# Performance work log

Hardware: AMD Instinct MI355X
Metric: run time of the kernel (lower is better)

## Reference

```python
import jax, jax.numpy as jnp
import numpy as np

R, H, E = 200000, 256, 100000  # num_relations, hidden_dim, num_hyperedges


def setup_inputs() -> dict:
    key = jax.random.key(0)
    ks = jax.random.split(key, 8)
    rng = np.random.default_rng(0)
    # ragged hyperedge sizes in [1, 15], avg ~8 -> total ~800k src entries
    sizes = rng.integers(1, 16, size=E)
    total = int(sizes.sum())
    he_ptr = jnp.asarray(np.concatenate([[0], np.cumsum(sizes)]), dtype=jnp.int64)
    he_src = jax.random.randint(ks[0], (total,), 0, R, dtype=jnp.int64)
    # unique targets make the scatter deterministic and equivalent)
    he_tgt = jnp.asarray(rng.permutation(R)[:E], dtype=jnp.int64)
    he_w = jax.random.uniform(ks[1], (E,), dtype=jnp.float32)
    x = jax.random.normal(ks[2], (R, H), dtype=jnp.float32)
    s = 1.0 / np.sqrt(H)
    W_msg = jax.random.uniform(ks[3], (H, H), jnp.float32, -s, s)
    b_msg = jnp.zeros((H,), jnp.float32)
    W_gate = jax.random.uniform(ks[4], (2 * H, H), jnp.float32, -s, s)
    b_gate = jnp.zeros((H,), jnp.float32)
    W_upd = jax.random.uniform(ks[5], (H, H), jnp.float32, -s, s)
    b_upd = jnp.zeros((H,), jnp.float32)
    return {"x": x, "he_ptr": he_ptr, "he_src": he_src, "he_tgt": he_tgt,
            "he_w": he_w, "W_msg": W_msg, "b_msg": b_msg,
            "W_gate": W_gate, "b_gate": b_gate, "W_upd": W_upd, "b_upd": b_upd}


def reference(x, he_ptr, he_src, he_tgt, he_w, W_msg, b_msg, W_gate, b_gate, W_upd, b_upd):
    total = he_src.shape[0]
    num_e = he_tgt.shape[0]
    # segment id of each src entry: which hyperedge it belongs to
    seg = jnp.searchsorted(he_ptr, jnp.arange(total), side="right") - 1
    gathered = x[he_src]                                   # [total, H]
    sums = jax.ops.segment_sum(gathered, seg, num_segments=num_e)  # [E, H]
    counts = (he_ptr[1:] - he_ptr[:-1]).astype(x.dtype)    # [E]
    src_mean = sums / counts[:, None]                      # segment mean
    msg = src_mean @ W_msg + b_msg                         # [E, H]
    tgt_x = x[he_tgt]                                      # [E, H]
    gate = jax.nn.sigmoid(jnp.concatenate([tgt_x, msg], axis=-1) @ W_gate + b_gate)
    upd = tgt_x + he_w[:, None] * gate * msg               # gated residual
    out = x.at[he_tgt].set(upd)                            # unique targets
    out = jnp.clip(out @ W_upd + b_upd, 0.0, 1.0)          # clipped relu
    return out
```

## Files before the change

kernel.cpp:

```cpp
#include <hip/hip_runtime.h>
#include <math.h>

#define H 256

typedef __attribute__((ext_vector_type(8))) short short8;
typedef __attribute__((ext_vector_type(4))) float f32x4;
typedef __attribute__((ext_vector_type(4))) int int4v;
typedef __attribute__((ext_vector_type(2))) unsigned int uint2v;
typedef unsigned short ushort_t;

__device__ __forceinline__ float bf2f(unsigned short u) {
    union { unsigned int i; float f; } v; v.i = ((unsigned int)u) << 16; return v.f;
}
__device__ __forceinline__ unsigned short f2bf(float f) {
    union { float f; unsigned int i; } v; v.f = f;
    unsigned int r = v.i + 0x7FFFu + ((v.i >> 16) & 1u);
    return (unsigned short)(r >> 16);
}
__device__ __forceinline__ void glds16(const void* g, void* l) {
    __builtin_amdgcn_global_load_lds((const __attribute__((address_space(1))) void*)g,
                                     (__attribute__((address_space(3))) void*)l, 16, 0, 0);
}
__device__ __forceinline__ int4v pack_f32x8_bf16(const float* p) {
    float4 f0 = *(const float4*)(p);
    float4 f1 = *(const float4*)(p + 4);
    int4v d;
    d.x = (int)((unsigned)f2bf(f0.x) | ((unsigned)f2bf(f0.y) << 16));
    d.y = (int)((unsigned)f2bf(f0.z) | ((unsigned)f2bf(f0.w) << 16));
    d.z = (int)((unsigned)f2bf(f1.x) | ((unsigned)f2bf(f1.y) << 16));
    d.w = (int)((unsigned)f2bf(f1.z) | ((unsigned)f2bf(f1.w) << 16));
    return d;
}

__global__ void prep_weights(const float* __restrict__ Wm, const float* __restrict__ Wg,
                             const float* __restrict__ Wu,
                             ushort_t* __restrict__ Wmt, ushort_t* __restrict__ Wgt,
                             ushort_t* __restrict__ Wut) {
    int idx = blockIdx.x * 256 + threadIdx.x;
    if (idx < 65536) {
        int n = idx >> 8, k = idx & 255;
        Wmt[idx] = f2bf(Wm[(size_t)k * 256 + n]);
        Wut[idx] = f2bf(Wu[(size_t)k * 256 + n]);
    }
    if (idx < 131072) {
        int n = idx >> 9, k = idx & 511;
        Wgt[idx] = f2bf(Wg[(size_t)k * 256 + n]);
    }
}

__global__ void imap_init(int* __restrict__ imap, int R) {
    int r = blockIdx.x * 256 + threadIdx.x;
    if (r < R) imap[r] = -1;
}
__global__ void imap_scatter(const int* __restrict__ tgt, int* __restrict__ imap, int E) {
    int e = blockIdx.x * 256 + threadIdx.x;
    if (e < E) imap[tgt[e]] = e;
}

__global__ void conv_bf16(const float* __restrict__ x, ushort_t* __restrict__ yb, size_t n8) {
    size_t i = (size_t)blockIdx.x * blockDim.x + threadIdx.x;
    size_t stride = (size_t)gridDim.x * blockDim.x;
    for (; i < n8; i += stride)
        *(int4v*)(yb + i * 8) = pack_f32x8_bf16(x + i * 8);
}

__global__ __launch_bounds__(256) void seg_mean_bf16(const ushort_t* __restrict__ yb,
                                                     const int* __restrict__ ptr,
                                                     const int* __restrict__ src,
                                                     ushort_t* __restrict__ smb, int E) {
    int e = blockIdx.x * 4 + (threadIdx.x >> 6);
    if (e >= E) return;
    int lane = threadIdx.x & 63;
    int s = ptr[e], t = ptr[e + 1];
    float a0 = 0.f, a1 = 0.f, a2 = 0.f, a3 = 0.f;
    int i = s;
    for (; i + 4 <= t; i += 4) {
        uint2v v0 = *(const uint2v*)(yb + (size_t)src[i + 0] * H + lane * 4);
        uint2v v1 = *(const uint2v*)(yb + (size_t)src[i + 1] * H + lane * 4);
        uint2v v2 = *(const uint2v*)(yb + (size_t)src[i + 2] * H + lane * 4);
        uint2v v3 = *(const uint2v*)(yb + (size_t)src[i + 3] * H + lane * 4);
        a0 += bf2f(v0.x & 0xffff) + bf2f(v1.x & 0xffff) + bf2f(v2.x & 0xffff) + bf2f(v3.x & 0xffff);
        a1 += bf2f(v0.x >> 16)    + bf2f(v1.x >> 16)    + bf2f(v2.x >> 16)    + bf2f(v3.x >> 16);
        a2 += bf2f(v0.y & 0xffff) + bf2f(v1.y & 0xffff) + bf2f(v2.y & 0xffff) + bf2f(v3.y & 0xffff);
        a3 += bf2f(v0.y >> 16)    + bf2f(v1.y >> 16)    + bf2f(v2.y >> 16)    + bf2f(v3.y >> 16);
    }
    for (; i < t; ++i) {
        uint2v v = *(const uint2v*)(yb + (size_t)src[i] * H + lane * 4);
        a0 += bf2f(v.x & 0xffff); a1 += bf2f(v.x >> 16);
        a2 += bf2f(v.y & 0xffff); a3 += bf2f(v.y >> 16);
    }
    float inv = 1.f / (float)(t - s);
    uint2v o;
    o.x = (unsigned)f2bf(a0 * inv) | ((unsigned)f2bf(a1 * inv) << 16);
    o.y = (unsigned)f2bf(a2 * inv) | ((unsigned)f2bf(a3 * inv) << 16);
    *(uint2v*)(smb + (size_t)e * H + lane * 4) = o;
}

__global__ __launch_bounds__(256) void seg_mean_f32w(const float* __restrict__ x,
                                                     const int* __restrict__ ptr,
                                                     const int* __restrict__ src,
                                                     ushort_t* __restrict__ smb, int E) {
    int e = blockIdx.x * 4 + (threadIdx.x >> 6);
    if (e >= E) return;
    int lane = threadIdx.x & 63;
    int s = ptr[e], t = ptr[e + 1];
    float a0 = 0.f, a1 = 0.f, a2 = 0.f, a3 = 0.f;
    int i = s;
    for (; i + 4 <= t; i += 4) {
        float4 v0 = *(const float4*)(x + (size_t)src[i + 0] * H + lane * 4);
        float4 v1 = *(const float4*)(x + (size_t)src[i + 1] * H + lane * 4);
        float4 v2 = *(const float4*)(x + (size_t)src[i + 2] * H + lane * 4);
        float4 v3 = *(const float4*)(x + (size_t)src[i + 3] * H + lane * 4);
        a0 += v0.x + v1.x + v2.x + v3.x;
        a1 += v0.y + v1.y + v2.y + v3.y;
        a2 += v0.z + v1.z + v2.z + v3.z;
        a3 += v0.w + v1.w + v2.w + v3.w;
    }
    for (; i < t; ++i) {
        float4 v = *(const float4*)(x + (size_t)src[i] * H + lane * 4);
        a0 += v.x; a1 += v.y; a2 += v.z; a3 += v.w;
    }
    float inv = 1.f / (float)(t - s);
    uint2v o;
    o.x = (unsigned)f2bf(a0 * inv) | ((unsigned)f2bf(a1 * inv) << 16);
    o.y = (unsigned)f2bf(a2 * inv) | ((unsigned)f2bf(a3 * inv) << 16);
    *(uint2v*)(smb + (size_t)e * H + lane * 4) = o;
}

template<int MODE, int KTOT, bool XB>
__global__ __launch_bounds__(256) void mfma_gemm(
    const ushort_t* __restrict__ Abf,
    const float* __restrict__ Xf,
    const ushort_t* __restrict__ Xb,
    const ushort_t* __restrict__ Aux,
    const int* __restrict__ Idx,
    const float* __restrict__ Hew,
    const ushort_t* __restrict__ Wt,
    const float* __restrict__ Bias,
    ushort_t* __restrict__ OutB,
    float* __restrict__ OutF,
    int M)
{
    constexpr int NT = KTOT / 32;
    const int m0 = blockIdx.x * 128;
    const int c0 = blockIdx.y * 128;
    const int tid = threadIdx.x;
    const int wv = tid >> 6;
    const int lane = tid & 63;
    const int wr = wv >> 1, wc = wv & 1;

    __shared__ __align__(16) ushort_t As[2][128 * 32];
    __shared__ __align__(16) ushort_t Bs[2][128 * 32];

    f32x4 acc[4][4];
#pragma unroll
    for (int i = 0; i < 4; ++i)
#pragma unroll
        for (int j = 0; j < 4; ++j) acc[i][j] = (f32x4){0.f, 0.f, 0.f, 0.f};

    const int ch0 = wv * 64 + lane;
    const int ch1 = ch0 + 256;

    auto stageB = [&](int buf, int k0) {
#pragma unroll
        for (int c = 0; c < 2; ++c) {
            int ch = c ? ch1 : ch0;
            int col = ch >> 2, sl = ch & 3, cc = sl ^ (col & 3);
            glds16(Wt + (size_t)(c0 + col) * KTOT + (k0 + cc * 8),
                   (char*)(&Bs[buf][0]) + ch * 16);
        }
    };

    auto stageA = [&](int buf, int k0) {
#pragma unroll
        for (int c = 0; c < 2; ++c) {
            int ch = c ? ch1 : ch0;
            int row = ch >> 2, sl = ch & 3, cc = sl ^ (row & 3);
            int kg = k0 + cc * 8;
            int r = m0 + row; if (r > M - 1) r = M - 1;
            if constexpr (MODE == 0) {
                glds16(Abf + (size_t)r * KTOT + kg, (char*)(&As[buf][0]) + ch * 16);
            } else {
                int4v d;
                if constexpr (MODE == 1) {
                    if (k0 < 256) {
                        int tr = Idx[r];
                        if constexpr (XB) d = *(const int4v*)(Xb + (size_t)tr * 256 + kg);
                        else              d = pack_f32x8_bf16(Xf + (size_t)tr * 256 + kg);
                    } else {
                        d = *(const int4v*)(Aux + (size_t)r * 256 + (kg - 256));
                    }
                } else {
                    int e = Idx[r];
                    if (e >= 0) d = *(const int4v*)(Aux + (size_t)e * 256 + kg);
                    else if constexpr (XB) d = *(const int4v*)(Xb + (size_t)r * 256 + kg);
                    else d = pack_f32x8_bf16(Xf + (size_t)r * 256 + kg);
                }
                *(int4v*)((char*)(&As[buf][0]) + ch * 16) = d;
            }
        }
    };

    auto compute = [&](int buf) {
        short8 a[4], b[4];
#pragma unroll
        for (int fm = 0; fm < 4; ++fm) {
            int row = wr * 64 + fm * 16 + (lane & 15);
            int byte = (row * 4 + ((lane >> 4) ^ (row & 3))) * 16;
            a[fm] = *(const short8*)((const char*)(&As[buf][0]) + byte);
        }
#pragma unroll
        for (int fn = 0; fn < 4; ++fn) {
            int col = wc * 64 + fn * 16 + (lane & 15);
            int byte = (col * 4 + ((lane >> 4) ^ (col & 3))) * 16;
            b[fn] = *(const short8*)((const char*)(&Bs[buf][0]) + byte);
        }
#pragma unroll
        for (int fm = 0; fm < 4; ++fm)
#pragma unroll
            for (int fn = 0; fn < 4; ++fn)
                acc[fm][fn] = __builtin_amdgcn_mfma_f32_16x16x32_bf16(a[fm], b[fn], acc[fm][fn], 0, 0, 0);
    };

    stageA(0, 0); stageB(0, 0);
    __syncthreads();
    for (int kt = 0; kt < NT; ++kt) {
        if (kt + 1 < NT) { stageA((kt + 1) & 1, (kt + 1) * 32); stageB((kt + 1) & 1, (kt + 1) * 32); }
        compute(kt & 1);
        __syncthreads();
    }

#pragma unroll
    for (int fm = 0; fm < 4; ++fm) {
        int rbase = m0 + wr * 64 + fm * 16 + (lane >> 4) * 4;
#pragma unroll
        for (int fn = 0; fn < 4; ++fn) {
            int col = c0 + wc * 64 + fn * 16 + (lane & 15);
            float bia = Bias[col];
            f32x4 v = acc[fm][fn];
#pragma unroll
            for (int i = 0; i < 4; ++i) {
                int rg = rbase + i;
                if (rg < M) {
                    float z = v[i] + bia;
                    if constexpr (MODE == 0) {
                        OutB[(size_t)rg * 256 + col] = f2bf(z);
                    } else if constexpr (MODE == 1) {
                        float g = 1.f / (1.f + __expf(-z));
                        int tr = Idx[rg];
                        float tx;
                        if constexpr (XB) tx = bf2f(Xb[(size_t)tr * 256 + col]);
                        else              tx = Xf[(size_t)tr * 256 + col];
                        float m = bf2f(Aux[(size_t)rg * 256 + col]);
                        float u = tx + Hew[rg] * g * m;
                        OutB[(size_t)rg * 256 + col] = f2bf(u);
                    } else {
                        OutF[(size_t)rg * 256 + col] = fminf(fmaxf(z, 0.f), 1.f);
                    }
                }
            }
        }
    }
}

extern "C" void kernel_launch(void* const* d_in, const int* in_sizes, int n_in,
                              void* d_out, int out_size, void* d_ws, size_t ws_size,
                              hipStream_t stream) {
    const float* x      = (const float*)d_in[0];
    const int*   he_ptr = (const int*)d_in[1];
    const int*   he_src = (const int*)d_in[2];
    const int*   he_tgt = (const int*)d_in[3];
    const float* he_w   = (const float*)d_in[4];
    const float* W_msg  = (const float*)d_in[5];
    const float* b_msg  = (const float*)d_in[6];
    const float* W_gate = (const float*)d_in[7];
    const float* b_gate = (const float*)d_in[8];
    const float* W_upd  = (const float*)d_in[9];
    const float* b_upd  = (const float*)d_in[10];

    const int E = in_sizes[3];
    const int R = in_sizes[0] / H;

    const size_t wbytes = (size_t)(65536 + 131072 + 65536) * 2;
    const size_t needA = (size_t)R * H * 2 + (size_t)E * H * 2 * 2 + (size_t)R * 4 + wbytes;
    const bool bigws = ws_size >= needA;

    dim3 gE((E + 127) / 128, 2);
    dim3 gR((R + 127) / 128, 2);

    if (bigws) {
        char* ws = (char*)d_ws;
        ushort_t* yb   = (ushort_t*)ws;
        ushort_t* buf0 = yb + (size_t)R * H;
        ushort_t* buf1 = buf0 + (size_t)E * H;
        int*      imap = (int*)(buf1 + (size_t)E * H);
        ushort_t* Wmt  = (ushort_t*)((char*)imap + (size_t)R * 4);
        ushort_t* Wgt  = Wmt + 256 * 256;
        ushort_t* Wut  = Wgt + 256 * 512;

        prep_weights<<<512, 256, 0, stream>>>(W_msg, W_gate, W_upd, Wmt, Wgt, Wut);
        imap_init<<<(R + 255) / 256, 256, 0, stream>>>(imap, R);
        imap_scatter<<<(E + 255) / 256, 256, 0, stream>>>(he_tgt, imap, E);
        conv_bf16<<<2048, 256, 0, stream>>>(x, yb, (size_t)R * H / 8);
        seg_mean_bf16<<<(E + 3) / 4, 256, 0, stream>>>(yb, he_ptr, he_src, buf0, E);

        mfma_gemm<0, 256, true><<<gE, 256, 0, stream>>>(buf0, nullptr, yb, nullptr, nullptr, nullptr,
                                                        Wmt, b_msg, buf1, nullptr, E);
        mfma_gemm<1, 512, true><<<gE, 256, 0, stream>>>(nullptr, nullptr, yb, buf1, he_tgt, he_w,
                                                        Wgt, b_gate, buf0, nullptr, E);
        mfma_gemm<2, 256, true><<<gR, 256, 0, stream>>>(nullptr, nullptr, yb, buf0, imap, nullptr,
                                                        Wut, b_upd, nullptr, (float*)d_out, R);
    } else {
        char* ws = (char*)d_ws;
        ushort_t* buf0 = (ushort_t*)ws;
        ushort_t* buf1 = buf0 + (size_t)E * H;
        int*      imap = (int*)(buf1 + (size_t)E * H);
        ushort_t* Wmt  = (ushort_t*)((char*)imap + (size_t)R * 4);
        ushort_t* Wgt  = Wmt + 256 * 256;
        ushort_t* Wut  = Wgt + 256 * 512;

        prep_weights<<<512, 256, 0, stream>>>(W_msg, W_gate, W_upd, Wmt, Wgt, Wut);
        imap_init<<<(R + 255) / 256, 256, 0, stream>>>(imap, R);
        imap_scatter<<<(E + 255) / 256, 256, 0, stream>>>(he_tgt, imap, E);
        seg_mean_f32w<<<(E + 3) / 4, 256, 0, stream>>>(x, he_ptr, he_src, buf0, E);

        mfma_gemm<0, 256, false><<<gE, 256, 0, stream>>>(buf0, nullptr, nullptr, nullptr, nullptr, nullptr,
                                                         Wmt, b_msg, buf1, nullptr, E);
        mfma_gemm<1, 512, false><<<gE, 256, 0, stream>>>(nullptr, x, nullptr, buf1, he_tgt, he_w,
                                                         Wgt, b_gate, buf0, nullptr, E);
        mfma_gemm<2, 256, false><<<gR, 256, 0, stream>>>(nullptr, x, nullptr, buf0, imap, nullptr,
                                                         Wut, b_upd, nullptr, (float*)d_out, R);
    }
}
```

Before: 422.1 us.

## Rewrite GEMMs as persistent weight-stationary kernels with LDS-resident weights

Replaces the double-buffered 128x128 tiled GEMM with a persistent kernel that loads the whole weight slice (up to 128 KB) into LDS once per block. Each wave then walks 16-row tiles, holding the A rows in registers and prefetching the next tile while computing. This removes the per-k-step syncthreads and the repeated weight staging. In exchange it uses large LDS and register budgets, which limits occupancy, and A fragments are read straight from global memory without coalesced staging.

```diff
diff --git a/kernel.cpp b/kernel.cpp
--- a/kernel.cpp
+++ b/kernel.cpp
@@ -127,8 +127,8 @@
     *(uint2v*)(smb + (size_t)e * H + lane * 4) = o;
 }
 
-template<int MODE, int KTOT, bool XB>
-__global__ __launch_bounds__(256) void mfma_gemm(
+template<int MODE, int KTOT, int NCOLS, bool XB>
+__global__ __launch_bounds__(512, 2) void wgemm(
     const ushort_t* __restrict__ Abf,
     const float* __restrict__ Xf,
     const ushort_t* __restrict__ Xb,
@@ -141,125 +141,163 @@
     float* __restrict__ OutF,
     int M)
 {
-    constexpr int NT = KTOT / 32;
-    const int m0 = blockIdx.x * 128;
-    const int c0 = blockIdx.y * 128;
+    constexpr int KS  = KTOT / 32;
+    constexpr int CT  = NCOLS / 16;
+    constexpr int CPR = KTOT / 8;
+    const int c0 = blockIdx.y * NCOLS;
     const int tid = threadIdx.x;
     const int wv = tid >> 6;
     const int lane = tid & 63;
-    const int wr = wv >> 1, wc = wv & 1;
-
-    __shared__ __align__(16) ushort_t As[2][128 * 32];
-    __shared__ __align__(16) ushort_t Bs[2][128 * 32];
-
-    f32x4 acc[4][4];
-#pragma unroll
-    for (int i = 0; i < 4; ++i)
-#pragma unroll
-        for (int j = 0; j < 4; ++j) acc[i][j] = (f32x4){0.f, 0.f, 0.f, 0.f};
-
-    const int ch0 = wv * 64 + lane;
-    const int ch1 = ch0 + 256;
-
-    auto stageB = [&](int buf, int k0) {
-#pragma unroll
-        for (int c = 0; c < 2; ++c) {
-            int ch = c ? ch1 : ch0;
-            int col = ch >> 2, sl = ch & 3, cc = sl ^ (col & 3);
-            glds16(Wt + (size_t)(c0 + col) * KTOT + (k0 + cc * 8),
-                   (char*)(&Bs[buf][0]) + ch * 16);
+
+    __shared__ __align__(16) ushort_t Ws[NCOLS * KTOT];
+
+    {
+        constexpr int TOT = NCOLS * CPR;
+        for (int base = wv * 64; base < TOT; base += 512) {
+            int id = base + lane;
+            int n = id / CPR, cs = id % CPR;
+            int cg = cs ^ (n & 7);
+            glds16(Wt + (size_t)(c0 + n) * KTOT + cg * 8, (char*)Ws + (size_t)id * 16);
+        }
+    }
+    __syncthreads();
+
+    float biasv[CT];
+#pragma unroll
+    for (int t = 0; t < CT; ++t) biasv[t] = Bias[c0 + t * 16 + (lane & 15)];
+
+    const int ntiles = (M + 15) >> 4;
+    const int stride = gridDim.x * 8;
+    int tile = blockIdx.x * 8 + wv;
+    if (tile >= ntiles) return;
+
+    const int arow = lane & 15;
+    const int kg = lane >> 4;
+
+    auto loadA = [&](int tl, short8* A) {
+        int r = tl * 16 + arow; if (r > M - 1) r = M - 1;
+        if constexpr (MODE == 0) {
+            const ushort_t* p = Abf + (size_t)r * KTOT + kg * 8;
+#pragma unroll
+            for (int kk = 0; kk < KS; ++kk) A[kk] = *(const short8*)(p + kk * 32);
+        } else if constexpr (MODE == 1) {
+            int tr = Idx[r];
+            if constexpr (XB) {
+                const ushort_t* p = Xb + (size_t)tr * 256 + kg * 8;
+#pragma unroll
+                for (int kk = 0; kk < 8; ++kk) A[kk] = *(const short8*)(p + kk * 32);
+            } else {
+                const float* p = Xf + (size_t)tr * 256 + kg * 8;
+#pragma unroll
+                for (int kk = 0; kk < 8; ++kk) { int4v d = pack_f32x8_bf16(p + kk * 32); A[kk] = *(short8*)&d; }
+            }
+            const ushort_t* q = Aux + (size_t)r * 256 + kg * 8;
+#pragma unroll
+            for (int kk = 0; kk < 8; ++kk) A[8 + kk] = *(const short8*)(q + kk * 32);
+        } else {
+            int e = Idx[r];
+            if constexpr (XB) {
+                const ushort_t* p = (e >= 0) ? (Aux + (size_t)e * 256) : (Xb + (size_t)r * 256);
+                p += kg * 8;
+#pragma unroll
+                for (int kk = 0; kk < KS; ++kk) A[kk] = *(const short8*)(p + kk * 32);
+            } else {
+                if (e >= 0) {
+                    const ushort_t* p = Aux + (size_t)e * 256 + kg * 8;
+#pragma unroll
+                    for (int kk = 0; kk < KS; ++kk) A[kk] = *(const short8*)(p + kk * 32);
+                } else {
+                    const float* p = Xf + (size_t)r * 256 + kg * 8;
+#pragma unroll
+                    for (int kk = 0; kk < KS; ++kk) { int4v d = pack_f32x8_bf16(p + kk * 32); A[kk] = *(short8*)&d; }
+                }
+            }
         }
     };
 
-    auto stageA = [&](int buf, int k0) {
-#pragma unroll
-        for (int c = 0; c < 2; ++c) {
-            int ch = c ? ch1 : ch0;
-            int row = ch >> 2, sl = ch & 3, cc = sl ^ (row & 3);
-            int kg = k0 + cc * 8;
-            int r = m0 + row; if (r > M - 1) r = M - 1;
-            if constexpr (MODE == 0) {
-                glds16(Abf + (size_t)r * KTOT + kg, (char*)(&As[buf][0]) + ch * 16);
+    auto computeEpi = [&](int tl, const short8* A) {
+        f32x4 acc[CT];
+#pragma unroll
+        for (int t = 0; t < CT; ++t) acc[t] = (f32x4){0.f, 0.f, 0.f, 0.f};
+#pragma unroll
+        for (int kk = 0; kk < KS; ++kk) {
+            short8 a = A[kk];
+            int cs = (kg + 4 * kk) ^ (lane & 7);
+#pragma unroll
+            for (int t = 0; t < CT; ++t) {
+                int n = arow + 16 * t;
+                short8 b = *(const short8*)((const char*)Ws + ((size_t)n * CPR + cs) * 16);
+                acc[t] = __builtin_amdgcn_mfma_f32_16x16x32_bf16(a, b, acc[t], 0, 0, 0);
+            }
+        }
+        int rbase = tl * 16 + (lane >> 4) * 4;
+        if constexpr (MODE == 0) {
+#pragma unroll
+            for (int t = 0; t < CT; ++t) {
+                int col = c0 + t * 16 + (lane & 15);
+#pragma unroll
+                for (int i = 0; i < 4; ++i) {
+                    int rg = rbase + i;
+                    if (rg < M) OutB[(size_t)rg * 256 + col] = f2bf(acc[t][i] + biasv[t]);
+                }
+            }
+        } else if constexpr (MODE == 1) {
+            int4v tg4; f32x4 hw4;
+            if (rbase + 3 < M) {
+                tg4 = *(const int4v*)(Idx + rbase);
+                hw4 = *(const f32x4*)(Hew + rbase);
             } else {
-                int4v d;
-                if constexpr (MODE == 1) {
-                    if (k0 < 256) {
-                        int tr = Idx[r];
-                        if constexpr (XB) d = *(const int4v*)(Xb + (size_t)tr * 256 + kg);
-                        else              d = pack_f32x8_bf16(Xf + (size_t)tr * 256 + kg);
-                    } else {
-                        d = *(const int4v*)(Aux + (size_t)r * 256 + (kg - 256));
+#pragma unroll
+                for (int i = 0; i < 4; ++i) {
+                    int rg = rbase + i < M ? rbase + i : M - 1;
+                    tg4[i] = Idx[rg]; hw4[i] = Hew[rg];
+                }
+            }
+#pragma unroll
+            for (int t = 0; t < CT; ++t) {
+                int col = c0 + t * 16 + (lane & 15);
+#pragma unroll
+                for (int i = 0; i < 4; ++i) {
+                    int rg = rbase + i;
+                    if (rg < M) {
+                        float z = acc[t][i] + biasv[t];
+                        float g = 1.f / (1.f + __expf(-z));
+                        float tx = XB ? bf2f(Xb[(size_t)tg4[i] * 256 + col])
+                                      : Xf[(size_t)tg4[i] * 256 + col];
+                        float m = bf2f(Aux[(size_t)rg * 256 + col]);
+                        OutB[(size_t)rg * 256 + col] = f2bf(tx + hw4[i] * g * m);
                     }
-                } else {
-                    int e = Idx[r];
-                    if (e >= 0) d = *(const int4v*)(Aux + (size_t)e * 256 + kg);
-                    else if constexpr (XB) d = *(const int4v*)(Xb + (size_t)r * 256 + kg);
-                    else d = pack_f32x8_bf16(Xf + (size_t)r * 256 + kg);
-                }
-                *(int4v*)((char*)(&As[buf][0]) + ch * 16) = d;
+                }
+            }
+        } else {
+#pragma unroll
+            for (int t = 0; t < CT; ++t) {
+                int col = c0 + t * 16 + (lane & 15);
+#pragma unroll
+                for (int i = 0; i < 4; ++i) {
+                    int rg = rbase + i;
+                    if (rg < M) {
+                        float z = acc[t][i] + biasv[t];
+                        OutF[(size_t)rg * 256 + col] = fminf(fmaxf(z, 0.f), 1.f);
+                    }
+                }
             }
         }
     };
 
-    auto compute = [&](int buf) {
-        short8 a[4], b[4];
-#pragma unroll
-        for (int fm = 0; fm < 4; ++fm) {
-            int row = wr * 64 + fm * 16 + (lane & 15);
-            int byte = (row * 4 + ((lane >> 4) ^ (row & 3))) * 16;
-            a[fm] = *(const short8*)((const char*)(&As[buf][0]) + byte);
-        }
-#pragma unroll
-        for (int fn = 0; fn < 4; ++fn) {
-            int col = wc * 64 + fn * 16 + (lane & 15);
-            int byte = (col * 4 + ((lane >> 4) ^ (col & 3))) * 16;
-            b[fn] = *(const short8*)((const char*)(&Bs[buf][0]) + byte);
-        }
-#pragma unroll
-        for (int fm = 0; fm < 4; ++fm)
-#pragma unroll
-            for (int fn = 0; fn < 4; ++fn)
-                acc[fm][fn] = __builtin_amdgcn_mfma_f32_16x16x32_bf16(a[fm], b[fn], acc[fm][fn], 0, 0, 0);
-    };
-
-    stageA(0, 0); stageB(0, 0);
-    __syncthreads();
-    for (int kt = 0; kt < NT; ++kt) {
-        if (kt + 1 < NT) { stageA((kt + 1) & 1, (kt + 1) * 32); stageB((kt + 1) & 1, (kt + 1) * 32); }
-        compute(kt & 1);
-        __syncthreads();
-    }
-
-#pragma unroll
-    for (int fm = 0; fm < 4; ++fm) {
-        int rbase = m0 + wr * 64 + fm * 16 + (lane >> 4) * 4;
-#pragma unroll
-        for (int fn = 0; fn < 4; ++fn) {
-            int col = c0 + wc * 64 + fn * 16 + (lane & 15);
-            float bia = Bias[col];
-            f32x4 v = acc[fm][fn];
-#pragma unroll
-            for (int i = 0; i < 4; ++i) {
-                int rg = rbase + i;
-                if (rg < M) {
-                    float z = v[i] + bia;
-                    if constexpr (MODE == 0) {
-                        OutB[(size_t)rg * 256 + col] = f2bf(z);
-                    } else if constexpr (MODE == 1) {
-                        float g = 1.f / (1.f + __expf(-z));
-                        int tr = Idx[rg];
-                        float tx;
-                        if constexpr (XB) tx = bf2f(Xb[(size_t)tr * 256 + col]);
-                        else              tx = Xf[(size_t)tr * 256 + col];
-                        float m = bf2f(Aux[(size_t)rg * 256 + col]);
-                        float u = tx + Hew[rg] * g * m;
-                        OutB[(size_t)rg * 256 + col] = f2bf(u);
-                    } else {
-                        OutF[(size_t)rg * 256 + col] = fminf(fmaxf(z, 0.f), 1.f);
-                    }
-                }
-            }
-        }
+    short8 A0[KS], A1[KS];
+    loadA(tile, A0);
+    while (true) {
+        int t1 = tile + stride;
+        if (t1 < ntiles) loadA(t1, A1);
+        computeEpi(tile, A0);
+        tile = t1;
+        if (tile >= ntiles) break;
+        int t2 = tile + stride;
+        if (t2 < ntiles) loadA(t2, A0);
+        computeEpi(tile, A1);
+        tile = t2;
+        if (tile >= ntiles) break;
     }
 }
 
@@ -285,9 +323,6 @@
     const size_t needA = (size_t)R * H * 2 + (size_t)E * H * 2 * 2 + (size_t)R * 4 + wbytes;
     const bool bigws = ws_size >= needA;
 
-    dim3 gE((E + 127) / 128, 2);
-    dim3 gR((R + 127) / 128, 2);
-
     if (bigws) {
         char* ws = (char*)d_ws;
         ushort_t* yb   = (ushort_t*)ws;
@@ -304,12 +339,12 @@
         conv_bf16<<<2048, 256, 0, stream>>>(x, yb, (size_t)R * H / 8);
         seg_mean_bf16<<<(E + 3) / 4, 256, 0, stream>>>(yb, he_ptr, he_src, buf0, E);
 
-        mfma_gemm<0, 256, true><<<gE, 256, 0, stream>>>(buf0, nullptr, yb, nullptr, nullptr, nullptr,
-                                                        Wmt, b_msg, buf1, nullptr, E);
-        mfma_gemm<1, 512, true><<<gE, 256, 0, stream>>>(nullptr, nullptr, yb, buf1, he_tgt, he_w,
-                                                        Wgt, b_gate, buf0, nullptr, E);
-        mfma_gemm<2, 256, true><<<gR, 256, 0, stream>>>(nullptr, nullptr, yb, buf0, imap, nullptr,
-                                                        Wut, b_upd, nullptr, (float*)d_out, R);
+        wgemm<0, 256, 256, true><<<dim3(256, 1), 512, 0, stream>>>(
+            buf0, nullptr, yb, nullptr, nullptr, nullptr, Wmt, b_msg, buf1, nullptr, E);
+        wgemm<1, 512, 128, true><<<dim3(256, 2), 512, 0, stream>>>(
+            nullptr, nullptr, yb, buf1, he_tgt, he_w, Wgt, b_gate, buf0, nullptr, E);
+        wgemm<2, 256, 256, true><<<dim3(256, 1), 512, 0, stream>>>(
+            nullptr, nullptr, yb, buf0, imap, nullptr, Wut, b_upd, nullptr, (float*)d_out, R);
     } else {
         char* ws = (char*)d_ws;
         ushort_t* buf0 = (ushort_t*)ws;
@@ -324,11 +359,11 @@
         imap_scatter<<<(E + 255) / 256, 256, 0, stream>>>(he_tgt, imap, E);
         seg_mean_f32w<<<(E + 3) / 4, 256, 0, stream>>>(x, he_ptr, he_src, buf0, E);
 
-        mfma_gemm<0, 256, false><<<gE, 256, 0, stream>>>(buf0, nullptr, nullptr, nullptr, nullptr, nullptr,
-                                                         Wmt, b_msg, buf1, nullptr, E);
-        mfma_gemm<1, 512, false><<<gE, 256, 0, stream>>>(nullptr, x, nullptr, buf1, he_tgt, he_w,
-                                                         Wgt, b_gate, buf0, nullptr, E);
-        mfma_gemm<2, 256, false><<<gR, 256, 0, stream>>>(nullptr, x, nullptr, buf0, imap, nullptr,
-                                                         Wut, b_upd, nullptr, (float*)d_out, R);
-    }
-}
+        wgemm<0, 256, 256, false><<<dim3(256, 1), 512, 0, stream>>>(
+            buf0, nullptr, nullptr, nullptr, nullptr, nullptr, Wmt, b_msg, buf1, nullptr, E);
+        wgemm<1, 512, 128, false><<<dim3(256, 2), 512, 0, stream>>>(
+            nullptr, x, nullptr, buf1, he_tgt, he_w, Wgt, b_gate, buf0, nullptr, E);
+        wgemm<2, 256, 256, false><<<dim3(256, 1), 512, 0, stream>>>(
+            nullptr, x, nullptr, buf0, imap, nullptr, Wut, b_upd, nullptr, (float*)d_out, R);
+    }
+}
```

Measured after the change: 817.0 us. +93.5%, slower.
